# Optimization experiments

Hardware: AMD Instinct MI355X
Metric: run time of the kernel (lower is better)

## Reference

```python
import jax, jax.numpy as jnp
import numpy as np

B, N, H, F = 256, 256, 256, 64   # batch, nodes, hidden, output
NNB = 4                          # neighbors per node (nns - 1)
HEADS = 3
S = 2 ** NNB - 1                 # nonempty subsets for Mobius Choquet
# MASK[s, i] = True iff neighbor i is in subset s (subsets 1..2^n-1)
MASK = jnp.asarray(np.array([[(s >> i) & 1 for i in range(NNB)] for s in range(1, S + 1)], dtype=bool))


def setup_inputs() -> dict:
    key = jax.random.key(0)
    ks = jax.random.split(key, 12)
    w = 0.02
    centers = jnp.arange(N, dtype=jnp.int64)[:, None]
    neigh = jax.random.randint(ks[11], (N, NNB), 0, N).astype(jnp.int64)
    local_edges = jnp.concatenate([centers, neigh], axis=1)[:, None, :]  # [N, 1, 5]
    return {
        "observation": jax.random.normal(ks[0], (B, N, H), jnp.float32),
        "action": jax.random.normal(ks[1], (B, N, H), jnp.float32),
        "V_W1": jax.random.normal(ks[2], (N, H, H), jnp.float32) * w,
        "V_b1": jnp.zeros((N, H), jnp.float32),
        "V_W2": jax.random.normal(ks[3], (N, H, F), jnp.float32) * w,
        "V_b2": jnp.zeros((N, F), jnp.float32),
        "A_W1": jax.random.normal(ks[4], (N, 2 * H, H), jnp.float32) * w,
        "A_b1": jnp.zeros((N, H), jnp.float32),
        "A_W2": jax.random.normal(ks[5], (N, H, F), jnp.float32) * w,
        "A_b2": jnp.zeros((N, F), jnp.float32),
        "chi_m": jax.random.normal(ks[6], (N, HEADS, S), jnp.float32) * w,
        "local_edges": local_edges,
    }


def _mmlp2(x, W1, b1, W2, b2):
    # per-node (multi) 2-layer MLP: first layer ReLU, second linear (act=False)
    h = jax.nn.relu(jnp.einsum('bni,nio->bno', x, W1) + b1)
    return jnp.einsum('bnh,nho->bno', h, W2) + b2


def reference(observation, action, V_W1, V_b1, V_W2, V_b2,
              A_W1, A_b1, A_W2, A_b2, chi_m, local_edges):
    V = _mmlp2(observation, V_W1, V_b1, V_W2, V_b2)                      # [B,N,F]
    A = _mmlp2(jnp.concatenate([observation, action], axis=-1),
               A_W1, A_b1, A_W2, A_b2)                                   # [B,N,F]
    Q = A + V                                                            # [B,N,F]
    centers = local_edges[:, 0, 0]        # [N]
    neigh = local_edges[:, 0, 1:]         # [N, NNB]
    # .data in torch -> detach the gathered neighbor Q-values
    Qn = jax.lax.stop_gradient(Q[:, neigh, :])                           # [B,N,NNB,F]
    # Mobius Choquet: min over each nonempty subset of neighbors
    masked = jnp.where(MASK[None, None, :, :, None], Qn[:, :, None, :, :], jnp.inf)
    mins = masked.min(axis=3)                                            # [B,N,S,F]
    chi = jnp.einsum('bnsf,nhs->bnf', mins, chi_m) / HEADS               # [B,N,F]
    return (chi + Q[:, centers, :]).mean(axis=-1)                        # [B,N]
```

## Files before the change

### kernel.cpp

```cpp
#include <hip/hip_runtime.h>
#include <cstddef>


#define BN 256
#define HD 256
#define FD 64
#define NHD (BN * HD)
#define XS 40

typedef _Float16 f16x8 __attribute__((ext_vector_type(8)));
typedef _Float16 f16x4 __attribute__((ext_vector_type(4)));
typedef float f32x4 __attribute__((ext_vector_type(4)));

#define BAR_LGKM()                                                         \
  asm volatile("s_waitcnt lgkmcnt(0)" ::: "memory");                       \
  __builtin_amdgcn_s_barrier();                                            \
  asm volatile("" ::: "memory");

__device__ __forceinline__ f16x8 pack8(const float v[8]) {
  f16x8 r;
#pragma unroll
  for (int i = 0; i < 8; ++i) r[i] = (_Float16)v[i];
  return r;
}

__device__ __forceinline__ void x_load(const float* xs0, const float* xs1, int n,
                                       int row0, int kt, int tid, float4 xr[2]) {
  int kOff = kt * 32;
  const float* xs = (kOff < 256) ? xs0 : xs1;
  int row = tid >> 2, c = (tid & 3) * 4;
  const float* p = xs + (size_t)(row0 + row) * NHD + n * HD + (kOff & 255) + c;
  xr[0] = *(const float4*)p;
  xr[1] = *(const float4*)(p + 16);
}
__device__ __forceinline__ void x_write(_Float16* Xl, int tid, const float4 xr[2]) {
  int row = tid >> 2, c = (tid & 3) * 4;
  f16x4 a, b;
  a[0] = (_Float16)xr[0].x; a[1] = (_Float16)xr[0].y;
  a[2] = (_Float16)xr[0].z; a[3] = (_Float16)xr[0].w;
  b[0] = (_Float16)xr[1].x; b[1] = (_Float16)xr[1].y;
  b[2] = (_Float16)xr[1].z; b[3] = (_Float16)xr[1].w;
  *(f16x4*)(Xl + row * XS + c) = a;
  *(f16x4*)(Xl + row * XS + c + 16) = b;
}

__device__ __forceinline__ void w1_load(const float* __restrict__ wb, float wf[4][8]) {
#pragma unroll
  for (int nf = 0; nf < 4; ++nf)
#pragma unroll
    for (int j = 0; j < 8; ++j) wf[nf][j] = wb[(size_t)j * HD + nf * 16];
}

__device__ __forceinline__ void g1_compute(const f16x8 b[4], const _Float16* Xl,
                                           int lrow, int lq, f32x4 acc[4][4]) {
#pragma unroll
  for (int m = 0; m < 4; ++m) {
    f16x8 a = *(const f16x8*)(Xl + (m * 16 + lrow) * XS + lq * 8);
#pragma unroll
    for (int nf = 0; nf < 4; ++nf)
      acc[m][nf] = __builtin_amdgcn_mfma_f32_16x16x32_f16(a, b[nf], acc[m][nf], 0, 0, 0);
  }
}

#define G1_STEP(KT, WFC)                                                     \
  {                                                                          \
    const int kt_ = (KT);                                                    \
    BAR_LGKM()                             \
    f16x8 bfr[4];                      \
    _Pragma("unroll") for (int nf = 0; nf < 4; ++nf) bfr[nf] = pack8(WFC[nf]); \
    if (kt_ + 2 < NK) w1_load(wb + (size_t)(kt_ + 2) * 32 * HD, WFC);        \
    if (kt_ + 1 < NK) x_load(xs0, xs1, n, row0, kt_ + 1, tid, xr);           \
    g1_compute(bfr, Xl, lrow, lq, acc);                                      \
    BAR_LGKM()                             \
    if (kt_ + 1 < NK) x_write(Xl, tid, xr);         \
  }

template <int NK>
__device__ __forceinline__ void run_gemm1(const float* xs0, const float* xs1,
                                          const float* __restrict__ Wg,
                                          int n, int row0, int tid, int lrow, int lq,
                                          int Nbase, _Float16* Xl, f32x4 acc[4][4]) {
  const float* wb = Wg + (size_t)(lq * 8) * HD + Nbase + lrow;
  float wfA[4][8], wfB[4][8];
  float4 xr[2];
  w1_load(wb, wfA);
  w1_load(wb + (size_t)32 * HD, wfB);
  x_load(xs0, xs1, n, row0, 0, tid, xr);
  x_write(Xl, tid, xr);
#pragma unroll 1
  for (int kt = 0; kt < NK; kt += 2) {
    G1_STEP(kt, wfA)
    G1_STEP(kt + 1, wfB)
  }
  BAR_LGKM()
}

__device__ __forceinline__ void w2_stage(const float* __restrict__ W2g, _Float16* Wl,
                                         int half, int w, int l) {
#pragma unroll
  for (int cg = 0; cg < 4; ++cg) {
    int khi = w * 4 + cg;
    const float* p = W2g + (size_t)(half * 128 + khi * 8) * FD + l;
    f16x8 v;
#pragma unroll
    for (int r = 0; r < 8; ++r) v[r] = (_Float16)p[(size_t)r * FD];
    *(f16x8*)(Wl + ((size_t)(khi * 64 + l)) * 8) = v;
  }
}

__device__ __forceinline__ void gemm2_branch(const f32x4 acc[4][4], f32x4 acc2[4],
                                             const float* __restrict__ W2g,
                                             const float* __restrict__ b1g,
                                             _Float16* Wl, _Float16* slab,
                                             int lrow, int lq, int Nbase, int w, int l) {
  float bv[4];
#pragma unroll
  for (int nf = 0; nf < 4; ++nf) bv[nf] = b1g[Nbase + nf * 16 + lrow];
  w2_stage(W2g, Wl, 0, w, l);
#pragma unroll
  for (int s = 0; s < 8; ++s) {
    if (w == (s >> 1)) {
#pragma unroll
      for (int m = 0; m < 4; ++m)
#pragma unroll
        for (int nf2 = 0; nf2 < 2; ++nf2) {
          const int nf = (s & 1) * 2 + nf2;
#pragma unroll
          for (int r = 0; r < 4; ++r)
            slab[(m * 16 + lq * 4 + r) * XS + nf2 * 16 + lrow] =
                (_Float16)fmaxf(acc[m][nf][r] + bv[nf], 0.f);
        }
    }
    BAR_LGKM();
    f16x8 a2 = *(const f16x8*)(slab + (w * 16 + lrow) * XS + lq * 8);
    f16x8 bb[4];
#pragma unroll
    for (int nf = 0; nf < 4; ++nf)
      bb[nf] = *(const f16x8*)(Wl + ((size_t)(((s & 3) * 4 + lq) * 64 + nf * 16 + lrow)) * 8);
#pragma unroll
    for (int nf = 0; nf < 4; ++nf)
      acc2[nf] = __builtin_amdgcn_mfma_f32_16x16x32_f16(a2, bb[nf], acc2[nf], 0, 0, 0);
    BAR_LGKM();
    if (s == 3) w2_stage(W2g, Wl, 1, w, l);
  }
}

__global__ __launch_bounds__(256, 2) void phase1_kernel(
    const float* __restrict__ obs, const float* __restrict__ act,
    const float* __restrict__ V_W1, const float* __restrict__ V_b1,
    const float* __restrict__ V_W2, const float* __restrict__ V_b2,
    const float* __restrict__ A_W1, const float* __restrict__ A_b1,
    const float* __restrict__ A_W2, const float* __restrict__ A_b2,
    float* __restrict__ Q) {
  __shared__ __align__(16) _Float16 Wl[8192];
  __shared__ __align__(16) _Float16 Xl[2560];

  int tid = threadIdx.x;
  int l = tid & 63, w = tid >> 6;
  int lrow = l & 15, lq = l >> 4;
  int Nbase = w * 64;
  int bid = blockIdx.x;
  int n = ((bid >> 5) << 3) | (bid & 7);
  int row0 = ((bid >> 3) & 3) * 64;

  f32x4 acc[4][4];
  f32x4 acc2[4];
#pragma unroll
  for (int j = 0; j < 4; ++j) acc2[j] = (f32x4){0.f, 0.f, 0.f, 0.f};

#pragma unroll
  for (int m = 0; m < 4; ++m)
#pragma unroll
    for (int nf = 0; nf < 4; ++nf) acc[m][nf] = (f32x4){0.f, 0.f, 0.f, 0.f};
  {
    const int NK = 8;
    const float* xs0 = obs; const float* xs1 = obs;
    const float* Wg = V_W1 + (size_t)n * HD * HD;
    run_gemm1<8>(xs0, xs1, Wg, n, row0, tid, lrow, lq, Nbase, Xl, acc);
  }
  gemm2_branch(acc, acc2, V_W2 + (size_t)n * HD * FD, V_b1 + n * HD,
               Wl, Xl, lrow, lq, Nbase, w, l);

#pragma unroll
  for (int m = 0; m < 4; ++m)
#pragma unroll
    for (int nf = 0; nf < 4; ++nf) acc[m][nf] = (f32x4){0.f, 0.f, 0.f, 0.f};
  {
    const float* xs0 = obs; const float* xs1 = act;
    const float* Wg = A_W1 + (size_t)n * 2 * HD * HD;
    run_gemm1<16>(xs0, xs1, Wg, n, row0, tid, lrow, lq, Nbase, Xl, acc);
  }
  gemm2_branch(acc, acc2, A_W2 + (size_t)n * HD * FD, A_b1 + n * HD,
               Wl, Xl, lrow, lq, Nbase, w, l);

  const float* vb2 = V_b2 + n * FD;
  const float* ab2 = A_b2 + n * FD;
#pragma unroll
  for (int nf = 0; nf < 4; ++nf) {
    int f = nf * 16 + lrow;
    float bias = vb2[f] + ab2[f];
#pragma unroll
    for (int rr = 0; rr < 4; ++rr) {
      int row = row0 + w * 16 + lq * 4 + rr;
      Q[(size_t)row * (BN * FD) + n * FD + f] = acc2[nf][rr] + bias;
    }
  }
}

__global__ __launch_bounds__(256) void phase2_kernel(const float* __restrict__ Q,
                                                     const float* __restrict__ chi_m,
                                                     const int* __restrict__ le,
                                                     float* __restrict__ out) {
  int b = blockIdx.x;
  int n = threadIdx.x;
  int step = (le[5] == 1) ? 1 : 2;
  const int* e = le + n * 5 * step;
  int c  = e[0 * step] & (BN - 1);
  int n0 = e[1 * step] & (BN - 1);
  int n1 = e[2 * step] & (BN - 1);
  int n2 = e[3 * step] & (BN - 1);
  int n3 = e[4 * step] & (BN - 1);
  const float* ch = chi_m + n * 45;
  float cm[15];
#pragma unroll
  for (int s = 0; s < 15; ++s) cm[s] = (ch[s] + ch[15 + s] + ch[30 + s]) * (1.f / 3.f);
  const float* qb = Q + (size_t)b * (BN * FD);
  const float* q0 = qb + n0 * FD;
  const float* q1 = qb + n1 * FD;
  const float* q2 = qb + n2 * FD;
  const float* q3 = qb + n3 * FD;
  const float* qc = qb + c * FD;
  float acc = 0.f;
#pragma unroll
  for (int f = 0; f < FD; f += 4) {
    float4 v0 = *(const float4*)(q0 + f);
    float4 v1 = *(const float4*)(q1 + f);
    float4 v2 = *(const float4*)(q2 + f);
    float4 v3 = *(const float4*)(q3 + f);
    float4 vc = *(const float4*)(qc + f);
    const float* p0 = (const float*)&v0;
    const float* p1 = (const float*)&v1;
    const float* p2 = (const float*)&v2;
    const float* p3 = (const float*)&v3;
    const float* pc = (const float*)&vc;
#pragma unroll
    for (int u = 0; u < 4; ++u) {
      float a = p0[u], bq = p1[u], cq = p2[u], d = p3[u];
      float m01 = fminf(a, bq), m02 = fminf(a, cq), m03 = fminf(a, d);
      float m12 = fminf(bq, cq), m13 = fminf(bq, d), m23 = fminf(cq, d);
      float m012 = fminf(m01, cq), m013 = fminf(m01, d);
      float m023 = fminf(m02, d),  m123 = fminf(m12, d);
      float m0123 = fminf(m01, m23);
      float chi = cm[0] * a   + cm[1] * bq   + cm[2] * m01  + cm[3] * cq
                + cm[4] * m02 + cm[5] * m12  + cm[6] * m012 + cm[7] * d
                + cm[8] * m03 + cm[9] * m13  + cm[10] * m013 + cm[11] * m23
                + cm[12] * m023 + cm[13] * m123 + cm[14] * m0123;
      acc += chi + pc[u];
    }
  }
  out[b * BN + n] = acc * (1.f / 64.f);
}

extern "C" void kernel_launch(void* const* d_in, const int* in_sizes, int n_in,
                              void* d_out, int out_size, void* d_ws, size_t ws_size,
                              hipStream_t stream) {
  (void)in_sizes; (void)n_in; (void)out_size; (void)ws_size;
  const float* obs  = (const float*)d_in[0];
  const float* act  = (const float*)d_in[1];
  const float* V_W1 = (const float*)d_in[2];
  const float* V_b1 = (const float*)d_in[3];
  const float* V_W2 = (const float*)d_in[4];
  const float* V_b2 = (const float*)d_in[5];
  const float* A_W1 = (const float*)d_in[6];
  const float* A_b1 = (const float*)d_in[7];
  const float* A_W2 = (const float*)d_in[8];
  const float* A_b2 = (const float*)d_in[9];
  const float* chim = (const float*)d_in[10];
  const int*   le   = (const int*)d_in[11];
  float* Q   = (float*)d_ws;
  float* out = (float*)d_out;

  phase1_kernel<<<dim3(1024), dim3(256), 0, stream>>>(obs, act, V_W1, V_b1, V_W2, V_b2,
                                                      A_W1, A_b1, A_W2, A_b2, Q);
  phase2_kernel<<<dim3(256), dim3(256), 0, stream>>>(Q, chim, le, out);
}
```

Measured before the change: 126.8 us.

## Process two K-tiles per barrier and stream W2 fragments through registers

The first GEMM loop now stages two X tiles in two LDS buffers and runs two K-steps per barrier pair, which halves the number of synchronisations and prefetches the next two tiles' X and W1 data in advance. The second GEMM no longer stages W2 in a dedicated LDS array. Each lane loads its W2 fragments straight from global memory into registers and prefetches the next block, and the hidden-activation slab is widened so one barrier pair covers a 64-column chunk. This cuts LDS use from about 21KB to 10KB and halves the barriers, at the cost of more live registers (two X prefetch sets and two W2 fragment sets), which could hurt occupancy or cause spills under the 2-blocks launch bound.

```diff
diff --git a/kernel.cpp b/kernel.cpp
--- a/kernel.cpp
+++ b/kernel.cpp
@@ -7,6 +7,7 @@
 #define FD 64
 #define NHD (BN * HD)
 #define XS 40
+#define SLS 72
 
 typedef _Float16 f16x8 __attribute__((ext_vector_type(8)));
 typedef _Float16 f16x4 __attribute__((ext_vector_type(4)));
@@ -62,86 +63,97 @@
   }
 }
 
-#define G1_STEP(KT, WFC)                                                     \
-  {                                                                          \
-    const int kt_ = (KT);                                                    \
-    BAR_LGKM()                             \
-    f16x8 bfr[4];                      \
-    _Pragma("unroll") for (int nf = 0; nf < 4; ++nf) bfr[nf] = pack8(WFC[nf]); \
-    if (kt_ + 2 < NK) w1_load(wb + (size_t)(kt_ + 2) * 32 * HD, WFC);        \
-    if (kt_ + 1 < NK) x_load(xs0, xs1, n, row0, kt_ + 1, tid, xr);           \
-    g1_compute(bfr, Xl, lrow, lq, acc);                                      \
-    BAR_LGKM()                             \
-    if (kt_ + 1 < NK) x_write(Xl, tid, xr);         \
-  }
-
 template <int NK>
 __device__ __forceinline__ void run_gemm1(const float* xs0, const float* xs1,
                                           const float* __restrict__ Wg,
                                           int n, int row0, int tid, int lrow, int lq,
-                                          int Nbase, _Float16* Xl, f32x4 acc[4][4]) {
+                                          int Nbase, _Float16* Xl0, _Float16* Xl1,
+                                          f32x4 acc[4][4]) {
   const float* wb = Wg + (size_t)(lq * 8) * HD + Nbase + lrow;
   float wfA[4][8], wfB[4][8];
-  float4 xr[2];
+  float4 xr0[2], xr1[2];
+  x_load(xs0, xs1, n, row0, 0, tid, xr0);
+  x_load(xs0, xs1, n, row0, 1, tid, xr1);
   w1_load(wb, wfA);
   w1_load(wb + (size_t)32 * HD, wfB);
-  x_load(xs0, xs1, n, row0, 0, tid, xr);
-  x_write(Xl, tid, xr);
+  x_write(Xl0, tid, xr0);
+  x_write(Xl1, tid, xr1);
 #pragma unroll 1
-  for (int kt = 0; kt < NK; kt += 2) {
-    G1_STEP(kt, wfA)
-    G1_STEP(kt + 1, wfB)
-  }
-  BAR_LGKM()
-}
-
-__device__ __forceinline__ void w2_stage(const float* __restrict__ W2g, _Float16* Wl,
-                                         int half, int w, int l) {
-#pragma unroll
-  for (int cg = 0; cg < 4; ++cg) {
-    int khi = w * 4 + cg;
-    const float* p = W2g + (size_t)(half * 128 + khi * 8) * FD + l;
-    f16x8 v;
-#pragma unroll
-    for (int r = 0; r < 8; ++r) v[r] = (_Float16)p[(size_t)r * FD];
-    *(f16x8*)(Wl + ((size_t)(khi * 64 + l)) * 8) = v;
-  }
+  for (int st = 0; st < NK / 2; ++st) {
+    BAR_LGKM()
+    f16x8 bA[4], bB[4];
+#pragma unroll
+    for (int nf = 0; nf < 4; ++nf) bA[nf] = pack8(wfA[nf]);
+#pragma unroll
+    for (int nf = 0; nf < 4; ++nf) bB[nf] = pack8(wfB[nf]);
+    if (st + 1 < NK / 2) {
+      x_load(xs0, xs1, n, row0, 2 * st + 2, tid, xr0);
+      x_load(xs0, xs1, n, row0, 2 * st + 3, tid, xr1);
+      w1_load(wb + (size_t)(2 * st + 2) * 32 * HD, wfA);
+      w1_load(wb + (size_t)(2 * st + 3) * 32 * HD, wfB);
+    }
+    g1_compute(bA, Xl0, lrow, lq, acc);
+    g1_compute(bB, Xl1, lrow, lq, acc);
+    BAR_LGKM()
+    if (st + 1 < NK / 2) {
+      x_write(Xl0, tid, xr0);
+      x_write(Xl1, tid, xr1);
+    }
+  }
+}
+
+__device__ __forceinline__ void w2_load(const float* __restrict__ W2g, int jb, int kf,
+                                        int lrow, int lq, float wf[4][8]) {
+  const float* p = W2g + (size_t)(jb * 64 + kf * 32 + lq * 8) * FD + lrow;
+#pragma unroll
+  for (int nf = 0; nf < 4; ++nf)
+#pragma unroll
+    for (int j = 0; j < 8; ++j) wf[nf][j] = p[(size_t)j * FD + nf * 16];
 }
 
 __device__ __forceinline__ void gemm2_branch(const f32x4 acc[4][4], f32x4 acc2[4],
                                              const float* __restrict__ W2g,
                                              const float* __restrict__ b1g,
-                                             _Float16* Wl, _Float16* slab,
-                                             int lrow, int lq, int Nbase, int w, int l) {
+                                             _Float16* slab, int lrow, int lq,
+                                             int Nbase, int w) {
   float bv[4];
 #pragma unroll
   for (int nf = 0; nf < 4; ++nf) bv[nf] = b1g[Nbase + nf * 16 + lrow];
-  w2_stage(W2g, Wl, 0, w, l);
-#pragma unroll
-  for (int s = 0; s < 8; ++s) {
-    if (w == (s >> 1)) {
+  float wf2A[4][8], wf2B[4][8];
+  w2_load(W2g, 0, 0, lrow, lq, wf2A);
+  w2_load(W2g, 0, 1, lrow, lq, wf2B);
+#pragma unroll
+  for (int jb = 0; jb < 4; ++jb) {
+    if (w == jb) {
 #pragma unroll
       for (int m = 0; m < 4; ++m)
 #pragma unroll
-        for (int nf2 = 0; nf2 < 2; ++nf2) {
-          const int nf = (s & 1) * 2 + nf2;
+        for (int nf = 0; nf < 4; ++nf)
 #pragma unroll
           for (int r = 0; r < 4; ++r)
-            slab[(m * 16 + lq * 4 + r) * XS + nf2 * 16 + lrow] =
+            slab[(m * 16 + lq * 4 + r) * SLS + nf * 16 + lrow] =
                 (_Float16)fmaxf(acc[m][nf][r] + bv[nf], 0.f);
-        }
-    }
-    BAR_LGKM();
-    f16x8 a2 = *(const f16x8*)(slab + (w * 16 + lrow) * XS + lq * 8);
-    f16x8 bb[4];
+    }
+    BAR_LGKM()
+    f16x8 bbA[4];
+#pragma unroll
+    for (int nf = 0; nf < 4; ++nf) bbA[nf] = pack8(wf2A[nf]);
+    f16x8 a0 = *(const f16x8*)(slab + (w * 16 + lrow) * SLS + lq * 8);
 #pragma unroll
     for (int nf = 0; nf < 4; ++nf)
-      bb[nf] = *(const f16x8*)(Wl + ((size_t)(((s & 3) * 4 + lq) * 64 + nf * 16 + lrow)) * 8);
+      acc2[nf] = __builtin_amdgcn_mfma_f32_16x16x32_f16(a0, bbA[nf], acc2[nf], 0, 0, 0);
+    f16x8 bbB[4];
+#pragma unroll
+    for (int nf = 0; nf < 4; ++nf) bbB[nf] = pack8(wf2B[nf]);
+    if (jb < 3) {
+      w2_load(W2g, jb + 1, 0, lrow, lq, wf2A);
+      w2_load(W2g, jb + 1, 1, lrow, lq, wf2B);
+    }
+    f16x8 a1 = *(const f16x8*)(slab + (w * 16 + lrow) * SLS + 32 + lq * 8);
 #pragma unroll
     for (int nf = 0; nf < 4; ++nf)
-      acc2[nf] = __builtin_amdgcn_mfma_f32_16x16x32_f16(a2, bb[nf], acc2[nf], 0, 0, 0);
-    BAR_LGKM();
-    if (s == 3) w2_stage(W2g, Wl, 1, w, l);
+      acc2[nf] = __builtin_amdgcn_mfma_f32_16x16x32_f16(a1, bbB[nf], acc2[nf], 0, 0, 0);
+    BAR_LGKM()
   }
 }
 
@@ -152,8 +164,10 @@
     const float* __restrict__ A_W1, const float* __restrict__ A_b1,
     const float* __restrict__ A_W2, const float* __restrict__ A_b2,
     float* __restrict__ Q) {
-  __shared__ __align__(16) _Float16 Wl[8192];
-  __shared__ __align__(16) _Float16 Xl[2560];
+  __shared__ __align__(16) _Float16 Xbuf[2 * 64 * XS];
+  _Float16* Xl0 = Xbuf;
+  _Float16* Xl1 = Xbuf + 64 * XS;
+  _Float16* slab = Xbuf;
 
   int tid = threadIdx.x;
   int l = tid & 63, w = tid >> 6;
@@ -172,26 +186,19 @@
   for (int m = 0; m < 4; ++m)
 #pragma unroll
     for (int nf = 0; nf < 4; ++nf) acc[m][nf] = (f32x4){0.f, 0.f, 0.f, 0.f};
-  {
-    const int NK = 8;
-    const float* xs0 = obs; const float* xs1 = obs;
-    const float* Wg = V_W1 + (size_t)n * HD * HD;
-    run_gemm1<8>(xs0, xs1, Wg, n, row0, tid, lrow, lq, Nbase, Xl, acc);
-  }
+  run_gemm1<8>(obs, obs, V_W1 + (size_t)n * HD * HD, n, row0, tid, lrow, lq,
+               Nbase, Xl0, Xl1, acc);
   gemm2_branch(acc, acc2, V_W2 + (size_t)n * HD * FD, V_b1 + n * HD,
-               Wl, Xl, lrow, lq, Nbase, w, l);
+               slab, lrow, lq, Nbase, w);
 
 #pragma unroll
   for (int m = 0; m < 4; ++m)
 #pragma unroll
     for (int nf = 0; nf < 4; ++nf) acc[m][nf] = (f32x4){0.f, 0.f, 0.f, 0.f};
-  {
-    const float* xs0 = obs; const float* xs1 = act;
-    const float* Wg = A_W1 + (size_t)n * 2 * HD * HD;
-    run_gemm1<16>(xs0, xs1, Wg, n, row0, tid, lrow, lq, Nbase, Xl, acc);
-  }
+  run_gemm1<16>(obs, act, A_W1 + (size_t)n * 2 * HD * HD, n, row0, tid, lrow, lq,
+                Nbase, Xl0, Xl1, acc);
   gemm2_branch(acc, acc2, A_W2 + (size_t)n * HD * FD, A_b1 + n * HD,
-               Wl, Xl, lrow, lq, Nbase, w, l);
+               slab, lrow, lq, Nbase, w);
 
   const float* vb2 = V_b2 + n * FD;
   const float* ab2 = A_b2 + n * FD;
```

New measurement: 147.3 us. 16.2% more time.
